# Performance work log

Measured on AMD Instinct MI355X. Metric: run time of the kernel, lower is better.

The kernel has to match this reference:

```python
import jax, jax.numpy as jnp
import numpy as np

TOPK = 3
RAT_S = 0.05


def conv4d(x, w, bs):
    """Faithful fused version of the looped Conv4d (stride=1, padding=1, l_k=3).

    x:  (b, c_in, l, d, h, w)
    w:  (c_out, c_in, l_k, d_k, h_k, w_k)  -- w[:, :, i] is the i-th Conv3d weight
    bs: (l_k, c_out)                        -- per-i Conv3d biases
    The torch loop computes out[f] = sum_i conv3d_i(x[f + i - l_k//2]) for valid
    frame indices, which is exactly a 4D cross-correlation; the bias of conv3d_i
    is added once per VALID i, so boundary frames get fewer bias terms.
    """
    out = jax.lax.conv_general_dilated(
        x, w, window_strides=(1, 1, 1, 1), padding=[(1, 1)] * 4,
        dimension_numbers=("NCABXY", "OIABXY", "NCABXY"))
    l_i = x.shape[2]
    l_k = w.shape[2]
    f = jnp.arange(l_i)
    j = f[:, None] + jnp.arange(l_k)[None, :] - l_k // 2  # source frame per (f, i)
    valid = ((j >= 0) & (j < l_i)).astype(x.dtype)        # (l, l_k)
    bias = valid @ bs                                     # (l, c_out)
    return out + bias.T[None, :, :, None, None, None]


def zero_window(x_aff, h, w, rat_s):
    """x_aff: (b, h*w, h, w). Suppress a Gaussian window centered at each
    channel's (r, c) source location."""
    dt = x_aff.dtype
    sr = jnp.asarray(h * rat_s, dt)
    sc = jnp.asarray(w * rat_s, dt)
    ind_r = jnp.arange(h, dtype=dt)
    ind_c = jnp.arange(w, dtype=dt)
    cent_r = jnp.repeat(jnp.arange(h), w).astype(dt)  # (h*w,)
    cent_c = jnp.tile(jnp.arange(w), h).astype(dt)    # (h*w,)
    gr = jnp.exp(-((ind_r[None, :] - cent_r[:, None]) ** 2) / (2 * sr ** 2))  # (hw, h)
    gc = jnp.exp(-((ind_c[None, :] - cent_c[:, None]) ** 2) / (2 * sc ** 2))  # (hw, w)
    g = 1.0 - gr[:, :, None] * gc[:, None, :]  # (hw, h, w)
    return x_aff * g[None]


def setup_inputs() -> dict:
    key = jax.random.key(0)
    k = jax.random.split(key, 5)
    b, c, h, w = 4, 256, 32, 32
    x = jax.random.normal(k[0], (b, c, h, w), dtype=jnp.float32)
    w1 = jax.random.normal(k[1], (16, 1, 3, 3, 3, 3), dtype=jnp.float32) * 0.2
    b1 = jax.random.normal(k[2], (3, 16), dtype=jnp.float32) * 0.05
    w2 = jax.random.normal(k[3], (1, 16, 3, 3, 3, 3), dtype=jnp.float32) * 0.1
    b2 = jax.random.normal(k[4], (3, 1), dtype=jnp.float32) * 0.05
    return {"x": x, "w1": w1, "b1": b1, "w2": w2, "b2": b2}


def reference(x, w1, b1, w2, b2):
    b, c, h1, ww1 = x.shape
    n = h1 * ww1
    # F.normalize over channel dim (p=2, eps=1e-12)
    xn = x / jnp.maximum(jnp.linalg.norm(x, axis=1, keepdims=True), 1e-12)
    q = xn.transpose(0, 2, 3, 1).reshape(b, n, c)      # (b, hw, c)
    kmat = xn.reshape(b, c, n)                          # (b, c, hw)
    aff = jnp.einsum("bnc,bcm->bnm", q, kmat)          # (b, hw, hw)
    aff = zero_window(aff.reshape(b, n, h1, ww1), h1, ww1, RAT_S)
    x_fc = aff.reshape(b, 1, h1, ww1, h1, ww1)
    y = conv4d(x_fc, w1, b1)                            # (b, 16, h1, w1, h2, w2)
    y = conv4d(y, w2, b2)                               # (b, 1,  h1, w1, h2, w2)
    xc = y.reshape(b, n, h1, ww1)                       # (b, hw, h2, w2)
    # top-k values along dim=-3 (the query/channel axis)
    vals = jax.lax.top_k(xc.transpose(0, 2, 3, 1), TOPK)[0]  # (b, h2, w2, k)
    return vals.transpose(0, 3, 1, 2)                   # (b, k, h2, w2)
```

## Files before the change

### kernel.cpp

```cpp
#include <hip/hip_runtime.h>

#define HW 1024
#define CCH 256


typedef _Float16 h2v __attribute__((ext_vector_type(2)));
typedef short bf16x8 __attribute__((ext_vector_type(8)));
typedef float f32x4 __attribute__((ext_vector_type(4)));

__device__ __forceinline__ float fdot2(unsigned a, unsigned b, float c) {
#if __has_builtin(__builtin_amdgcn_fdot2)
    return __builtin_amdgcn_fdot2(__builtin_bit_cast(h2v, a),
                                  __builtin_bit_cast(h2v, b), c, false);
#else
    h2v ha = __builtin_bit_cast(h2v, a), hb = __builtin_bit_cast(h2v, b);
    return c + (float)ha.x * (float)hb.x + (float)ha.y * (float)hb.y;
#endif
}
__device__ __forceinline__ unsigned packh2(float x, float y) {
    h2v h;
    h.x = (_Float16)x;
    h.y = (_Float16)y;
    return __builtin_bit_cast(unsigned, h);
}
__device__ __forceinline__ unsigned short f2bf(float f) {
    unsigned u = __float_as_uint(f);
    u += 0x7fffu + ((u >> 16) & 1u);
    return (unsigned short)(u >> 16);
}

__global__ __launch_bounds__(256) void norm_kernel(const float* __restrict__ x,
                                                   unsigned short* __restrict__ xnT) {
    __shared__ float red[16][17];
    __shared__ float invs[16];
    int b = blockIdx.y;
    int p0 = blockIdx.x * 16;
    int cg = threadIdx.x >> 4;
    int pp = threadIdx.x & 15;
    int p = p0 + pp;
    const float* xb = x + (size_t)b * CCH * HW;
    float ss = 0.f;
#pragma unroll
    for (int i = 0; i < 16; ++i) {
        float v = xb[(size_t)(cg * 16 + i) * HW + p];
        ss += v * v;
    }
    red[cg][pp] = ss;
    __syncthreads();
    if (threadIdx.x < 16) {
        float s = 0.f;
#pragma unroll
        for (int g = 0; g < 16; ++g) s += red[g][threadIdx.x];
        invs[threadIdx.x] = 1.0f / fmaxf(sqrtf(s), 1e-12f);
    }
    __syncthreads();
    float inv = invs[pp];
    unsigned* o = (unsigned*)(xnT + ((size_t)b * HW + p) * CCH) + cg * 8;
#pragma unroll
    for (int i = 0; i < 8; ++i) {
        int c = cg * 16 + 2 * i;
        unsigned lo = f2bf(xb[(size_t)c * HW + p] * inv);
        unsigned hi = f2bf(xb[(size_t)(c + 1) * HW + p] * inv);
        o[i] = lo | (hi << 16);
    }
}

__global__ __launch_bounds__(256) void aff_kernel(const unsigned short* __restrict__ xnT,
                                                  unsigned short* __restrict__ Af16) {
    int b = blockIdx.z;
    int p0 = blockIdx.y * 64, m0 = blockIdx.x * 64;
    const unsigned short* X = xnT + (size_t)b * HW * CCH;
    int lane = threadIdx.x & 63, w = threadIdx.x >> 6;
    int pw = p0 + (w >> 1) * 32, mw = m0 + (w & 1) * 32;
    int lr = lane & 15, lg = lane >> 4;
    f32x4 acc[2][2] = {};
    for (int ks = 0; ks < 8; ++ks) {
        int kc = ks * 32 + lg * 8;
        bf16x8 a0 = *(const bf16x8*)&X[(size_t)(pw + lr) * CCH + kc];
        bf16x8 a1 = *(const bf16x8*)&X[(size_t)(pw + 16 + lr) * CCH + kc];
        bf16x8 b0 = *(const bf16x8*)&X[(size_t)(mw + lr) * CCH + kc];
        bf16x8 b1 = *(const bf16x8*)&X[(size_t)(mw + 16 + lr) * CCH + kc];
        acc[0][0] = __builtin_amdgcn_mfma_f32_16x16x32_bf16(a0, b0, acc[0][0], 0, 0, 0);
        acc[0][1] = __builtin_amdgcn_mfma_f32_16x16x32_bf16(a0, b1, acc[0][1], 0, 0, 0);
        acc[1][0] = __builtin_amdgcn_mfma_f32_16x16x32_bf16(a1, b0, acc[1][0], 0, 0, 0);
        acc[1][1] = __builtin_amdgcn_mfma_f32_16x16x32_bf16(a1, b1, acc[1][1], 0, 0, 0);
    }
#pragma unroll
    for (int pi = 0; pi < 2; ++pi)
#pragma unroll
        for (int mi = 0; mi < 2; ++mi)
#pragma unroll
            for (int r = 0; r < 4; ++r) {
                int p = pw + 16 * pi + lg * 4 + r;
                int m = mw + 16 * mi + lr;
                int dr = (m >> 5) - (p >> 5);
                int dc = (m & 31) - (p & 31);
                float gg = 1.0f - __expf(-(float)(dr * dr + dc * dc) * 0.1953125f);
                float v = acc[pi][mi][r] * gg;
                Af16[((size_t)b * HW + p) * HW + m] =
                    __builtin_bit_cast(unsigned short, (_Float16)v);
            }
}

__global__ __launch_bounds__(256) void g_kernel(const float* __restrict__ w1,
                                                const float* __restrict__ w2,
                                                float* __restrict__ G) {
    __shared__ float w1s[1296], w2s[1296];
    int tid = threadIdx.x;
    for (int i = tid; i < 1296; i += 256) { w1s[i] = w1[i]; w2s[i] = w2[i]; }
    __syncthreads();
    int idx = blockIdx.x * 256 + tid;
    if (idx < 6561) {
        int o1 = idx / 81, o2 = idx - o1 * 81;
        float s = 0.f;
#pragma unroll
        for (int ch = 0; ch < 16; ++ch) s += w1s[ch * 81 + o1] * w2s[ch * 81 + o2];
        G[idx] = s;
    }
}

__global__ __launch_bounds__(128) void wcomp_kernel(const float* __restrict__ G,
                                                    unsigned* __restrict__ Wpk) {
    __shared__ float Gs[6561];
    int cls = blockIdx.x;
    int t = threadIdx.x;
    for (int i = t; i < 6561; i += 128) Gs[i] = G[i];
    if (t < 25) Wpk[cls * 400 + t * 16 + 15] = 0u;
    __syncthreads();
    if (t >= 125) return;
    int a = t / 25, b_ = (t / 5) % 5, c = t % 5;
    int r1c = cls / 27, c1c = (cls / 9) % 3, r2c = (cls / 3) % 3, c2c = cls % 3;
    float W[5] = {};
    for (int i2 = 0; i2 < 3; ++i2) {
        if ((r1c == 0 && i2 == 0) || (r1c == 2 && i2 == 2)) continue;
        int i1 = a - i2;
        if (i1 < 0 || i1 > 2) continue;
        for (int j2 = 0; j2 < 3; ++j2) {
            if ((c1c == 0 && j2 == 0) || (c1c == 2 && j2 == 2)) continue;
            int j1 = b_ - j2;
            if (j1 < 0 || j1 > 2) continue;
            for (int u2 = 0; u2 < 3; ++u2) {
                if ((r2c == 0 && u2 == 0) || (r2c == 2 && u2 == 2)) continue;
                int u1 = c - u2;
                if (u1 < 0 || u1 > 2) continue;
                for (int v2 = 0; v2 < 3; ++v2) {
                    if ((c2c == 0 && v2 == 0) || (c2c == 2 && v2 == 2)) continue;
                    int o2 = i2 * 27 + j2 * 9 + u2 * 3 + v2;
                    int o1b = i1 * 27 + j1 * 9 + u1 * 3;
#pragma unroll
                    for (int d = 0; d < 5; ++d) {
                        int v1 = d - v2;
                        if (v1 < 0 || v1 > 2) continue;
                        W[d] += Gs[(o1b + v1) * 81 + o2];
                    }
                }
            }
        }
    }
    unsigned* o = &Wpk[cls * 400 + (a * 5 + b_) * 16 + c * 3];
    o[0] = packh2(W[0], W[1]);
    o[1] = packh2(W[2], W[3]);
    o[2] = packh2(W[4], 0.f);
}

__global__ __launch_bounds__(1024) void bt_kernel(const float* __restrict__ w2,
                                                  const float* __restrict__ b1,
                                                  const float* __restrict__ b2,
                                                  float* __restrict__ BT) {
    __shared__ float w2s[1296], b1s[48], S0[81], S1[81], S2[81];
    int t = threadIdx.x;
    for (int i = t; i < 1296; i += 1024) w2s[i] = w2[i];
    if (t < 48) b1s[t] = b1[t];
    __syncthreads();
    if (t < 81) {
        float s0 = 0.f, s1 = 0.f, s2 = 0.f;
#pragma unroll
        for (int ch = 0; ch < 16; ++ch) {
            float w = w2s[ch * 81 + t];
            s0 += w * b1s[16 + ch];
            s1 += w * b1s[ch];
            s2 += w * b1s[32 + ch];
        }
        S0[t] = s0; S1[t] = s1; S2[t] = s2;
    }
    __syncthreads();
    if (t >= 864) return;
    int r1 = t / 27, c1c = (t / 9) % 3, r2c = (t / 3) % 3, c2c = t % 3;
    float s = b2[1] + (r1 >= 1 ? b2[0] : 0.f) + (r1 <= 30 ? b2[2] : 0.f);
    for (int i2 = 0; i2 < 3; ++i2) {
        int rr = r1 + i2 - 1;
        if (rr < 0 || rr > 31) continue;
        float m1 = (rr >= 1) ? 1.f : 0.f, m2 = (rr <= 30) ? 1.f : 0.f;
        for (int j2 = 0; j2 < 3; ++j2) {
            if ((c1c == 0 && j2 == 0) || (c1c == 2 && j2 == 2)) continue;
            for (int u2 = 0; u2 < 3; ++u2) {
                if ((r2c == 0 && u2 == 0) || (r2c == 2 && u2 == 2)) continue;
                for (int v2 = 0; v2 < 3; ++v2) {
                    if ((c2c == 0 && v2 == 0) || (c2c == 2 && v2 == 2)) continue;
                    int o2 = i2 * 27 + j2 * 9 + u2 * 3 + v2;
                    s += S0[o2] + m1 * S1[o2] + m2 * S2[o2];
                }
            }
        }
    }
    BT[t] = s;
}

#define HSD 56
__global__ __launch_bounds__(64) void convc_kernel(const unsigned short* __restrict__ Af16,
                                                   const unsigned* __restrict__ Wpk,
                                                   const float* __restrict__ BT,
                                                   float* __restrict__ xc) {
    __shared__ unsigned halo[36 * HSD];
    int tid = threadIdx.x;
    int P = blockIdx.x, b = blockIdx.y;
    int r1 = P >> 5, c1 = P & 31;
    int r1c = (r1 == 0) ? 0 : (r1 == 31) ? 2 : 1;
    int c1c = (c1 == 0) ? 0 : (c1 == 31) ? 2 : 1;

    const uint4* wsrc = (const uint4*)(Wpk + (size_t)((r1c * 3 + c1c) * 9 + 4) * 400);
    float bias = BT[r1 * 27 + c1c * 9 + 4];

    for (int i = tid; i < 36 * HSD; i += 64) halo[i] = 0;

    int qr2 = tid >> 2;
    int qc = tid & 3;
    int srow = tid >> 1;
    int st = tid & 1;
    int wbase = (srow + 2) * HSD + 8 * st + 1;

    const uint4* Ab4 = (const uint4*)(Af16 + (size_t)b * HW * HW);

    float acc0[8] = {}, acc1[8] = {};

    int pr0 = min(max(r1 - 2, 0), 31), pc0 = min(max(c1 - 2, 0), 31);
    uint4 pfA = Ab4[(size_t)(pr0 * 32 + pc0) * 128 + 2 * tid];
    uint4 pfB = Ab4[(size_t)(pr0 * 32 + pc0) * 128 + 2 * tid + 1];

    __syncthreads();

#pragma unroll 1
    for (int tp = 0; tp < 25; ++tp) {
        int tr = tp / 5, tc = tp - tr * 5;
        int apr = r1 + tr - 2, apc = c1 + tc - 2;
        bool valid = ((unsigned)apr < 32u) && ((unsigned)apc < 32u);
        uint4 curA = pfA, curB = pfB;
        if (tp < 24) {
            int t2 = tp + 1;
            int tr2 = t2 / 5, tc2 = t2 - tr2 * 5;
            int npr = min(max(r1 + tr2 - 2, 0), 31);
            int npc = min(max(c1 + tc2 - 2, 0), 31);
            pfA = Ab4[(size_t)(npr * 32 + npc) * 128 + 2 * tid];
            pfB = Ab4[(size_t)(npr * 32 + npc) * 128 + 2 * tid + 1];
        }
        if (!valid) continue;

        uint4 w4a = wsrc[tp * 4 + 0];
        uint4 w4b = wsrc[tp * 4 + 1];
        uint4 w4c = wsrc[tp * 4 + 2];
        uint4 w4d = wsrc[tp * 4 + 3];

        __syncthreads();
        {
            unsigned* hb = &halo[wbase];
            hb[0] = curA.x; hb[1] = curA.y; hb[2] = curA.z; hb[3] = curA.w;
            hb[4] = curB.x; hb[5] = curB.y; hb[6] = curB.z; hb[7] = curB.w;
        }
        __syncthreads();

        unsigned wr[16] = {w4a.x, w4a.y, w4a.z, w4a.w, w4b.x, w4b.y, w4b.z, w4b.w,
                           w4c.x, w4c.y, w4c.z, w4c.w, w4d.x, w4d.y, w4d.z, w4d.w};
        const unsigned* base = &halo[(2 * qr2) * HSD + 4 * qc];
#pragma unroll
        for (int i = 0; i < 6; ++i) {
            const unsigned* rp = base + i * HSD;
            uint2 e0 = *(const uint2*)rp;
            uint2 e1 = *(const uint2*)(rp + 2);
            uint2 e2 = *(const uint2*)(rp + 4);
            unsigned q0 = e0.x, q1 = e0.y, q2 = e1.x, q3 = e1.y, q4 = e2.x, q5 = e2.y;
            unsigned pp[12];
            pp[0] = q0;  pp[2] = q1;  pp[4] = q2;  pp[6] = q3;  pp[8] = q4;  pp[10] = q5;
            pp[1] = (q0 >> 16) | (q1 << 16);
            pp[3] = (q1 >> 16) | (q2 << 16);
            pp[5] = (q2 >> 16) | (q3 << 16);
            pp[7] = (q3 >> 16) | (q4 << 16);
            pp[9] = (q4 >> 16) | (q5 << 16);
            pp[11] = (q5 >> 16);
            if (i <= 4) {
                unsigned wa = wr[i * 3], wb_ = wr[i * 3 + 1], wc_ = wr[i * 3 + 2];
#pragma unroll
                for (int cc = 0; cc < 8; ++cc) {
                    float a = acc0[cc];
                    a = fdot2(wa, pp[cc], a);
                    a = fdot2(wb_, pp[cc + 2], a);
                    a = fdot2(wc_, pp[cc + 4], a);
                    acc0[cc] = a;
                }
            }
            if (i >= 1) {
                int u = i - 1;
                unsigned wa = wr[u * 3], wb_ = wr[u * 3 + 1], wc_ = wr[u * 3 + 2];
#pragma unroll
                for (int cc = 0; cc < 8; ++cc) {
                    float a = acc1[cc];
                    a = fdot2(wa, pp[cc], a);
                    a = fdot2(wb_, pp[cc + 2], a);
                    a = fdot2(wc_, pp[cc + 4], a);
                    acc1[cc] = a;
                }
            }
        }
    }

    float* xp = &xc[((size_t)b * HW + P) * HW];
    int o0 = (2 * qr2) * 32 + 8 * qc;
    int o1 = (2 * qr2 + 1) * 32 + 8 * qc;
    *(float4*)&xp[o0] = make_float4(acc0[0] + bias, acc0[1] + bias, acc0[2] + bias, acc0[3] + bias);
    *(float4*)&xp[o0 + 4] = make_float4(acc0[4] + bias, acc0[5] + bias, acc0[6] + bias, acc0[7] + bias);
    *(float4*)&xp[o1] = make_float4(acc1[0] + bias, acc1[1] + bias, acc1[2] + bias, acc1[3] + bias);
    *(float4*)&xp[o1 + 4] = make_float4(acc1[4] + bias, acc1[5] + bias, acc1[6] + bias, acc1[7] + bias);
}

__global__ __launch_bounds__(256) void expand_kernel(const unsigned short* __restrict__ Af16,
                                                     unsigned* __restrict__ Apad32) {
    int plane = blockIdx.x, b = blockIdx.y;
    const unsigned* src = (const unsigned*)(Af16 + ((size_t)b * HW + plane) * HW);
    unsigned* dst = Apad32 + ((size_t)b * HW + plane) * 720;
    for (int k = threadIdx.x; k < 720; k += 256) {
        int pr = k / 20, pcd = k - pr * 20;
        unsigned val = 0;
        if (pr >= 2 && pr < 34 && pcd >= 1 && pcd <= 16)
            val = src[(pr - 2) * 16 + (pcd - 1)];
        dst[k] = val;
    }
}

__global__ __launch_bounds__(128) void fix_kernel(const unsigned* __restrict__ Apad32,
                                                  const unsigned* __restrict__ Wpk,
                                                  const float* __restrict__ BT,
                                                  float* __restrict__ xc) {
    __shared__ __align__(16) unsigned wl[3600];
    __shared__ float bts[9];
    int tid = threadIdx.x;
    int P = blockIdx.x, b = blockIdx.y;
    int r1 = P >> 5, c1 = P & 31;
    int r1c = (r1 == 0) ? 0 : (r1 == 31) ? 2 : 1;
    int c1c = (c1 == 0) ? 0 : (c1 == 31) ? 2 : 1;

    const unsigned* wsrc = Wpk + (size_t)(r1c * 3 + c1c) * 3600;
    for (int i = tid; i < 3600; i += 128) wl[i] = wsrc[i];
    if (tid < 9) bts[tid] = BT[r1 * 27 + c1c * 9 + tid];

    int li = tid;
    bool act = li < 124;
    int qr, qc;
    if (li < 32) { qr = 0; qc = li; }
    else if (li < 64) { qr = 31; qc = li - 32; }
    else if (li < 94) { qr = li - 63; qc = 0; }
    else { qr = min(li, 123) - 93; qc = 31; }
    int r2c = (qr == 0) ? 0 : (qr == 31) ? 2 : 1;
    int c2c = (qc == 0) ? 0 : (qc == 31) ? 2 : 1;
    int v = r2c * 3 + c2c;
    int sh = (qc & 1) * 16;
    int sd = qc >> 1;

    __syncthreads();
    float acc = 0.f;

#pragma unroll 1
    for (int tp = 0; tp < 25; ++tp) {
        int tr = tp / 5, tc = tp - tr * 5;
        int apr = r1 + tr - 2, apc = c1 + tc - 2;
        if ((unsigned)apr >= 32u || (unsigned)apc >= 32u) continue;
        const unsigned* tpl = Apad32 + ((size_t)b * HW + apr * 32 + apc) * 720;
        const uint4* wv4 = (const uint4*)&wl[v * 400 + tp * 16];
        uint4 wa = wv4[0], wb = wv4[1], wc2 = wv4[2], wd = wv4[3];
        unsigned wr[16] = {wa.x, wa.y, wa.z, wa.w, wb.x, wb.y, wb.z, wb.w,
                           wc2.x, wc2.y, wc2.z, wc2.w, wd.x, wd.y, wd.z, wd.w};
#pragma unroll
        for (int u = 0; u < 5; ++u) {
            const unsigned* rp = tpl + (qr + u) * 20 + sd;
            unsigned d0 = rp[0], d1 = rp[1], d2 = rp[2];
            unsigned pa = __builtin_amdgcn_alignbit(d1, d0, sh);
            unsigned pb = __builtin_amdgcn_alignbit(d2, d1, sh);
            unsigned pc_ = __builtin_amdgcn_alignbit(0u, d2, sh);
            acc = fdot2(wr[u * 3 + 0], pa, acc);
            acc = fdot2(wr[u * 3 + 1], pb, acc);
            acc = fdot2(wr[u * 3 + 2], pc_, acc);
        }
    }

    if (act)
        xc[((size_t)b * HW + P) * HW + qr * 32 + qc] = acc + bts[v];
}

__device__ __forceinline__ void top3_push(float v, float& t0, float& t1, float& t2) {
    float n0 = fminf(t0, v);
    t0 = fmaxf(t0, v);
    float n1 = fminf(t1, n0);
    t1 = fmaxf(t1, n0);
    t2 = fmaxf(t2, n1);
}

__global__ __launch_bounds__(256) void topk1_kernel(const float* __restrict__ xc,
                                                    float* __restrict__ part) {
    int q = blockIdx.x * 256 + threadIdx.x;
    int pc = blockIdx.y, bi = blockIdx.z;
    float t0 = -1e30f, t1 = -1e30f, t2 = -1e30f;
    const float* xp = xc + (size_t)bi * HW * HW;
    for (int p = pc * 32; p < pc * 32 + 32; ++p)
        top3_push(xp[(size_t)p * HW + q], t0, t1, t2);
    float* pp = part + (size_t)(bi * 32 + pc) * 3 * HW;
    pp[q] = t0;
    pp[HW + q] = t1;
    pp[2 * HW + q] = t2;
}

__global__ __launch_bounds__(256) void topk2_kernel(const float* __restrict__ part,
                                                    float* __restrict__ out) {
    int q = blockIdx.x * 256 + threadIdx.x;
    int bi = blockIdx.y;
    float t0 = -1e30f, t1 = -1e30f, t2 = -1e30f;
    const float* pp = part + (size_t)bi * 96 * HW;
    for (int k = 0; k < 96; ++k) top3_push(pp[(size_t)k * HW + q], t0, t1, t2);
    float* ob = out + (size_t)bi * 3 * HW;
    ob[q] = t0;
    ob[HW + q] = t1;
    ob[2 * HW + q] = t2;
}

extern "C" void kernel_launch(void* const* d_in, const int* in_sizes, int n_in,
                              void* d_out, int out_size, void* d_ws, size_t ws_size,
                              hipStream_t stream) {
    const float* x = (const float*)d_in[0];
    const float* w1 = (const float*)d_in[1];
    const float* b1 = (const float*)d_in[2];
    const float* w2 = (const float*)d_in[3];
    const float* b2 = (const float*)d_in[4];
    float* out = (float*)d_out;
    float* ws = (float*)d_ws;

    unsigned short* xnT = (unsigned short*)ws;
    unsigned short* Af16 = (unsigned short*)(ws + 524288);
    float* xc = ws + 2621440;
    unsigned* Wpk = (unsigned*)(ws + 6815744);
    float* BT = ws + 6848512;
    float* part = ws + 6849536;
    unsigned* Apad32 = (unsigned*)(ws + 7242752);
    float* G = ws + 10191872;

    norm_kernel<<<dim3(64, 4), 256, 0, stream>>>(x, xnT);
    aff_kernel<<<dim3(16, 16, 4), 256, 0, stream>>>(xnT, Af16);
    expand_kernel<<<dim3(1024, 4), 256, 0, stream>>>(Af16, Apad32);
    g_kernel<<<26, 256, 0, stream>>>(w1, w2, G);
    wcomp_kernel<<<81, 128, 0, stream>>>(G, Wpk);
    bt_kernel<<<1, 1024, 0, stream>>>(w2, b1, b2, BT);
    convc_kernel<<<dim3(1024, 4), 64, 0, stream>>>(Af16, Wpk, BT, xc);
    fix_kernel<<<dim3(1024, 4), 128, 0, stream>>>(Apad32, Wpk, BT, xc);
    topk1_kernel<<<dim3(4, 32, 4), 256, 0, stream>>>(xc, part);
    topk2_kernel<<<dim3(4, 4), 256, 0, stream>>>(part, out);
}
```

Measured before the change: 178.0 us.

## Pack four output positions per block in convc and remap thread-to-halo indexing

convc_kernel now runs 256 threads per block, with each 64-lane wavefront handling its own output position and its own shared halo buffer, so the grid shrinks fourfold. The thread-to-element mapping changes: staging writes go to row = lane&31 with two halves, compute reads use qr2 = lane&15 and qc = lane>>4, and the halo stride grows to 66 to change LDS bank behavior. Because __syncthreads now spans four waves that may disagree on validity, the invalid-tap skip is moved after the barriers. The block-wide barriers couple independent waves and may add stalls, and the larger shared footprint can lower occupancy.

```diff
diff --git a/kernel.cpp b/kernel.cpp
--- a/kernel.cpp
+++ b/kernel.cpp
@@ -206,14 +206,16 @@
     BT[t] = s;
 }
 
-#define HSD 56
-__global__ __launch_bounds__(64) void convc_kernel(const unsigned short* __restrict__ Af16,
-                                                   const unsigned* __restrict__ Wpk,
-                                                   const float* __restrict__ BT,
-                                                   float* __restrict__ xc) {
-    __shared__ unsigned halo[36 * HSD];
+#define HSD 66
+__global__ __launch_bounds__(256) void convc_kernel(const unsigned short* __restrict__ Af16,
+                                                    const unsigned* __restrict__ Wpk,
+                                                    const float* __restrict__ BT,
+                                                    float* __restrict__ xc) {
+    __shared__ unsigned halo[4][36 * HSD];
     int tid = threadIdx.x;
-    int P = blockIdx.x, b = blockIdx.y;
+    int w = tid >> 6, lane = tid & 63;
+    int P = blockIdx.x * 4 + w;
+    int b = blockIdx.y;
     int r1 = P >> 5, c1 = P & 31;
     int r1c = (r1 == 0) ? 0 : (r1 == 31) ? 2 : 1;
     int c1c = (c1 == 0) ? 0 : (c1 == 31) ? 2 : 1;
@@ -221,23 +223,21 @@
     const uint4* wsrc = (const uint4*)(Wpk + (size_t)((r1c * 3 + c1c) * 9 + 4) * 400);
     float bias = BT[r1 * 27 + c1c * 9 + 4];
 
-    for (int i = tid; i < 36 * HSD; i += 64) halo[i] = 0;
-
-    int qr2 = tid >> 2;
-    int qc = tid & 3;
-    int srow = tid >> 1;
-    int st = tid & 1;
-    int wbase = (srow + 2) * HSD + 8 * st + 1;
+    unsigned* myh = halo[w];
+    for (int i = lane; i < 36 * HSD; i += 64) myh[i] = 0;
+
+    int qr2 = lane & 15, qc = lane >> 4;
+    int srow = lane & 31, sth = lane >> 5;
+    int wbase = (srow + 2) * HSD + 8 * sth + 1;
+    int idx4 = srow * 4 + sth * 2;
 
     const uint4* Ab4 = (const uint4*)(Af16 + (size_t)b * HW * HW);
 
     float acc0[8] = {}, acc1[8] = {};
 
     int pr0 = min(max(r1 - 2, 0), 31), pc0 = min(max(c1 - 2, 0), 31);
-    uint4 pfA = Ab4[(size_t)(pr0 * 32 + pc0) * 128 + 2 * tid];
-    uint4 pfB = Ab4[(size_t)(pr0 * 32 + pc0) * 128 + 2 * tid + 1];
-
-    __syncthreads();
+    uint4 pfA = Ab4[(size_t)(pr0 * 32 + pc0) * 128 + idx4];
+    uint4 pfB = Ab4[(size_t)(pr0 * 32 + pc0) * 128 + idx4 + 1];
 
 #pragma unroll 1
     for (int tp = 0; tp < 25; ++tp) {
@@ -250,10 +250,9 @@
             int tr2 = t2 / 5, tc2 = t2 - tr2 * 5;
             int npr = min(max(r1 + tr2 - 2, 0), 31);
             int npc = min(max(c1 + tc2 - 2, 0), 31);
-            pfA = Ab4[(size_t)(npr * 32 + npc) * 128 + 2 * tid];
-            pfB = Ab4[(size_t)(npr * 32 + npc) * 128 + 2 * tid + 1];
-        }
-        if (!valid) continue;
+            pfA = Ab4[(size_t)(npr * 32 + npc) * 128 + idx4];
+            pfB = Ab4[(size_t)(npr * 32 + npc) * 128 + idx4 + 1];
+        }
 
         uint4 w4a = wsrc[tp * 4 + 0];
         uint4 w4b = wsrc[tp * 4 + 1];
@@ -261,16 +260,17 @@
         uint4 w4d = wsrc[tp * 4 + 3];
 
         __syncthreads();
-        {
-            unsigned* hb = &halo[wbase];
+        if (valid) {
+            unsigned* hb = &myh[wbase];
             hb[0] = curA.x; hb[1] = curA.y; hb[2] = curA.z; hb[3] = curA.w;
             hb[4] = curB.x; hb[5] = curB.y; hb[6] = curB.z; hb[7] = curB.w;
         }
         __syncthreads();
+        if (!valid) continue;
 
         unsigned wr[16] = {w4a.x, w4a.y, w4a.z, w4a.w, w4b.x, w4b.y, w4b.z, w4b.w,
                            w4c.x, w4c.y, w4c.z, w4c.w, w4d.x, w4d.y, w4d.z, w4d.w};
-        const unsigned* base = &halo[(2 * qr2) * HSD + 4 * qc];
+        const unsigned* base = &myh[(2 * qr2) * HSD + 4 * qc];
 #pragma unroll
         for (int i = 0; i < 6; ++i) {
             const unsigned* rp = base + i * HSD;
@@ -455,7 +455,7 @@
     g_kernel<<<26, 256, 0, stream>>>(w1, w2, G);
     wcomp_kernel<<<81, 128, 0, stream>>>(G, Wpk);
     bt_kernel<<<1, 1024, 0, stream>>>(w2, b1, b2, BT);
-    convc_kernel<<<dim3(1024, 4), 64, 0, stream>>>(Af16, Wpk, BT, xc);
+    convc_kernel<<<dim3(256, 4), 256, 0, stream>>>(Af16, Wpk, BT, xc);
     fix_kernel<<<dim3(1024, 4), 128, 0, stream>>>(Apad32, Wpk, BT, xc);
     topk1_kernel<<<dim3(4, 32, 4), 256, 0, stream>>>(xc, part);
     topk2_kernel<<<dim3(4, 4), 256, 0, stream>>>(part, out);
```

Result: no change. 175.1 us (-1.6%).
